# Kernel optimization log

Measured on AMD Instinct MI355X. Metric: run time of the kernel, lower is better.

## Reference

```python
import math
import jax, jax.numpy as jnp
import numpy as np

N, T, D, H, DH = 4, 2048, 1024, 16, 64
CAP = 30.0
EPS = 1e-5


def _layernorm(x, g, b):
    m = jnp.mean(x, axis=-1, keepdims=True)
    v = jnp.mean(jnp.square(x - m), axis=-1, keepdims=True)
    return (x - m) * jax.lax.rsqrt(v + EPS) * g + b


def _rope(x):
    # x: [N, H, t, d]; interleaved rotary (rotary-embedding-torch style), theta=10000
    t, d = x.shape[2], x.shape[3]
    inv_freq = 1.0 / (10000.0 ** (jnp.arange(0, d, 2, dtype=jnp.float32) / d))
    ang = jnp.arange(t, dtype=jnp.float32)[:, None] * inv_freq[None, :]  # [t, d/2]
    cos, sin = jnp.cos(ang), jnp.sin(ang)
    x1, x2 = x[..., 0::2], x[..., 1::2]
    r1 = x1 * cos - x2 * sin
    r2 = x1 * sin + x2 * cos
    return jnp.stack([r1, r2], axis=-1).reshape(x.shape)


def setup_inputs() -> dict:
    key = jax.random.key(0)
    ks = jax.random.split(key, 8)
    s = 0.02
    lengths = jax.random.randint(ks[6], (N,), T // 2, T + 1).astype(jnp.int32)
    key_padding_mask = jnp.arange(T)[None, :] >= lengths[:, None]  # True = pad
    attn_mask = jnp.triu(jnp.ones((T, T), dtype=bool), 1)  # causal: True = masked
    return {
        "x": jax.random.normal(ks[0], (N, T, D), jnp.float32),
        "ln_g": jnp.ones((D,), jnp.float32),
        "ln_b": jnp.zeros((D,), jnp.float32),
        "Wq": jax.random.normal(ks[1], (D, H * DH), jnp.float32) * s,
        "bq": jnp.zeros((H * DH,), jnp.float32),
        "Wk": jax.random.normal(ks[2], (D, H * DH), jnp.float32) * s,
        "bk": jnp.zeros((H * DH,), jnp.float32),
        "Wv": jax.random.normal(ks[3], (D, H * DH), jnp.float32) * s,
        "bv": jnp.zeros((H * DH,), jnp.float32),
        "Wo": jax.random.normal(ks[4], (H * DH, D), jnp.float32) * s,
        "bo": jnp.zeros((D,), jnp.float32),
        "key_padding_mask": key_padding_mask,
        "attn_mask": attn_mask,
        "key_value_sequence_lengths": lengths,
    }


def reference(x, ln_g, ln_b, Wq, bq, Wk, bk, Wv, bv, Wo, bo,
              key_padding_mask, attn_mask, key_value_sequence_lengths):
    n, t, _ = x.shape
    h = _layernorm(x, ln_g, ln_b)  # shared LN for q/k/v (self-attention)
    q = (h @ Wq + bq).reshape(n, t, H, DH).transpose(0, 2, 1, 3)  # [n,H,t,d]
    k = (h @ Wk + bk).reshape(n, t, H, DH).transpose(0, 2, 1, 3)
    v = (h @ Wv + bv).reshape(n, t, H, DH).transpose(0, 2, 1, 3)
    q = _rope(q)
    k = _rope(k)
    scores = jnp.einsum('bhtd,bhTd->bhtT', q, k) / math.sqrt(DH)
    scores = CAP * jnp.tanh(scores / CAP)  # tanh soft-cap
    mask = key_padding_mask[:, None, None, :] | attn_mask[None, None, :, :]
    scores = jnp.where(mask, -jnp.inf, scores)
    attn = jax.nn.softmax(scores, axis=-1)
    out = jnp.einsum('bhtT,bhTd->bhtd', attn, v)
    out = out.transpose(0, 2, 1, 3).reshape(n, t, H * DH)
    return out @ Wo + bo
```

## Files before the change

### kernel.cpp

```cpp
#include <hip/hip_runtime.h>
#include <hip/hip_bf16.h>

typedef unsigned short u16;
typedef unsigned int   u32;
typedef __bf16 bf16x8 __attribute__((ext_vector_type(8)));
typedef float  f32x4  __attribute__((ext_vector_type(4)));

#define NB 4
#define T_ 2048
#define D_ 1024
#define H_ 16
#define DH 64
#define M_ (NB * T_)
#define PSTR 72

__device__ __forceinline__ float bf2f(u16 u) {
    union { u32 i; float f; } v; v.i = ((u32)u) << 16; return v.f;
}
__device__ __forceinline__ u16 f2bf(float f) {
    union { float fl; u32 i; } v; v.fl = f;
    u32 r = v.i + 0x7fff + ((v.i >> 16) & 1);
    return (u16)(r >> 16);
}

__device__ __forceinline__ void gl_lds16(const u16* g, u16* l) {
    __builtin_amdgcn_global_load_lds((const __attribute__((address_space(1))) void*)g,
                                     (__attribute__((address_space(3))) void*)l,
                                     16, 0, 0);
}

__device__ __forceinline__ int detect_f32(const u16* p) {
    int weird = 0;
    const int lane = threadIdx.x & 63;
    #pragma unroll
    for (int i = 0; i < 4; ++i) {
        const u16 u = p[lane * 4 + i];
        const int e = (u >> 7) & 0xFF;
        weird += (e == 0xFF || (e >= 0x01 && e <= 0x3F) || (e >= 0xC0 && e <= 0xFE));
    }
    #pragma unroll
    for (int off = 32; off; off >>= 1) weird += __shfl_xor(weird, off);
    return weird >= 16;
}

__device__ __forceinline__ int read_len(const void* raw, int b) {
    const int* a32 = (const int*)raw;
    bool ok32 = true;
    #pragma unroll
    for (int i = 0; i < NB; ++i) {
        const int v = a32[i];
        if (v < 1 || v > T_) ok32 = false;
    }
    int v = ok32 ? a32[b] : (int)((const long long*)raw)[b];
    return min(max(v, 1), T_);
}

__global__ __launch_bounds__(256) void ln_kernel(const void* __restrict__ xraw,
                                                 const void* __restrict__ graw,
                                                 const void* __restrict__ braw,
                                                 u16* __restrict__ h) {
    const int row = blockIdx.x;
    const int tid = threadIdx.x;
    const int isf = detect_f32((const u16*)xraw);

    float xv[4];
    if (isf) {
        const float* xr = (const float*)xraw + (size_t)row * D_;
        *(float4*)xv = *(const float4*)&xr[tid * 4];
    } else {
        const u16* xr = (const u16*)xraw + (size_t)row * D_;
        u16 loc[4] __attribute__((aligned(8)));
        *(uint2*)loc = *(const uint2*)&xr[tid * 4];
        #pragma unroll
        for (int i = 0; i < 4; ++i) xv[i] = bf2f(loc[i]);
    }

    float s = xv[0] + xv[1] + xv[2] + xv[3];
    float q = xv[0]*xv[0] + xv[1]*xv[1] + xv[2]*xv[2] + xv[3]*xv[3];

    #pragma unroll
    for (int off = 32; off; off >>= 1) {
        s += __shfl_xor(s, off);
        q += __shfl_xor(q, off);
    }
    __shared__ float red[8];
    const int wave = tid >> 6, lane = tid & 63;
    if (lane == 0) { red[wave] = s; red[4 + wave] = q; }
    __syncthreads();
    s = red[0] + red[1] + red[2] + red[3];
    q = red[4] + red[5] + red[6] + red[7];

    const float mean = s * (1.0f / D_);
    const float var  = q * (1.0f / D_) - mean * mean;
    const float rs   = rsqrtf(var + 1e-5f);

    u16 o[4] __attribute__((aligned(8)));
    #pragma unroll
    for (int i = 0; i < 4; ++i) {
        const int c = tid * 4 + i;
        const float gv = isf ? ((const float*)graw)[c] : bf2f(((const u16*)graw)[c]);
        const float bv = isf ? ((const float*)braw)[c] : bf2f(((const u16*)braw)[c]);
        o[i] = f2bf((xv[i] - mean) * rs * gv + bv);
    }
    *(uint2*)&h[(size_t)row * D_ + tid * 4] = *(uint2*)o;
}

__global__ __launch_bounds__(256) void wconv_kernel(const void* __restrict__ Wraw,
                                                    u16* __restrict__ Wt) {
    __shared__ u16 tile[64][PSTR];
    const int isf = detect_f32((const u16*)Wraw);
    const int n0 = blockIdx.x * 64;
    const int k0 = blockIdx.y * 64;
    const int tid = threadIdx.x;
    const int tr  = tid >> 2;
    const int tc  = (tid & 3) * 16;

    if (isf) {
        const float* W = (const float*)Wraw;
        #pragma unroll
        for (int i = 0; i < 16; ++i)
            tile[tc + i][tr] = f2bf(W[(size_t)(k0 + tr) * D_ + n0 + tc + i]);
    } else {
        const u16* W = (const u16*)Wraw;
        #pragma unroll
        for (int i = 0; i < 16; ++i)
            tile[tc + i][tr] = W[(size_t)(k0 + tr) * D_ + n0 + tc + i];
    }
    __syncthreads();
    *(uint4*)&Wt[(size_t)(n0 + tr) * D_ + k0 + tc]     = *(uint4*)&tile[tr][tc];
    *(uint4*)&Wt[(size_t)(n0 + tr) * D_ + k0 + tc + 8] = *(uint4*)&tile[tr][tc + 8];
}

__global__ __launch_bounds__(256) void qkv_kernel(const u16* __restrict__ A,
                                                  const u16* __restrict__ Wt3,
                                                  const void* __restrict__ Braw,
                                                  const void* __restrict__ bqr,
                                                  const void* __restrict__ bkr,
                                                  const void* __restrict__ bvr,
                                                  u16* __restrict__ qo,
                                                  u16* __restrict__ ko,
                                                  u16* __restrict__ vo) {
    __shared__ __align__(16) u16 As[128 * 32];
    __shared__ __align__(16) u16 Bs[128 * 32];

    const int tid   = threadIdx.x;
    const int wave  = tid >> 6;
    const int lane  = tid & 63;
    const int quad  = lane >> 4;
    const int lr    = lane & 15;
    const int ntile = blockIdx.x * 128;
    const int mtile = blockIdx.y * 128;
    const int seg   = ntile >> 10;

    const int isf = detect_f32((const u16*)Braw);

    const int srow = wave * 32 + (lane >> 2);
    const int scol = (lane & 3) * 8;
    const u16* aptr0 = A   + (size_t)(mtile + srow) * D_ + scol;
    const u16* aptr1 = A   + (size_t)(mtile + srow + 16) * D_ + scol;
    const u16* bptr0 = Wt3 + (size_t)(ntile + srow) * D_ + scol;
    const u16* bptr1 = Wt3 + (size_t)(ntile + srow + 16) * D_ + scol;
    u16* alds0 = As + wave * 1024;
    u16* alds1 = As + wave * 1024 + 512;
    u16* blds0 = Bs + wave * 1024;
    u16* blds1 = Bs + wave * 1024 + 512;

    const int mbase = (wave >> 1) * 64;
    const int nbase = (wave & 1) * 64;

    f32x4 acc[4][4];
    #pragma unroll
    for (int m = 0; m < 4; ++m)
        #pragma unroll
        for (int n = 0; n < 4; ++n)
            acc[m][n] = (f32x4){0.f, 0.f, 0.f, 0.f};

    for (int k0 = 0; k0 < D_; k0 += 32) {
        gl_lds16(aptr0 + k0, alds0);
        gl_lds16(aptr1 + k0, alds1);
        gl_lds16(bptr0 + k0, blds0);
        gl_lds16(bptr1 + k0, blds1);
        __syncthreads();

        bf16x8 af[4], bfr[4];
        #pragma unroll
        for (int m = 0; m < 4; ++m)
            af[m] = *(const bf16x8*)&As[(mbase + m * 16 + lr) * 32 + quad * 8];
        #pragma unroll
        for (int n = 0; n < 4; ++n)
            bfr[n] = *(const bf16x8*)&Bs[(nbase + n * 16 + lr) * 32 + quad * 8];
        #pragma unroll
        for (int m = 0; m < 4; ++m)
            #pragma unroll
            for (int n = 0; n < 4; ++n)
                acc[m][n] = __builtin_amdgcn_mfma_f32_16x16x32_bf16(af[m], bfr[n], acc[m][n], 0, 0, 0);

        __syncthreads();
    }

    const void* biasraw = (seg == 0) ? bqr : (seg == 1) ? bkr : bvr;
    u16* out            = (seg == 0) ? qo  : (seg == 1) ? ko  : vo;
    const int nloc = (ntile & 1023) + nbase;

    #pragma unroll
    for (int m = 0; m < 4; ++m) {
        #pragma unroll
        for (int n = 0; n < 4; ++n) {
            const int ncl = nloc + n * 16 + lr;
            const float bv = isf ? ((const float*)biasraw)[ncl]
                                 : bf2f(((const u16*)biasraw)[ncl]);
            #pragma unroll
            for (int r = 0; r < 4; ++r) {
                const int mrow = mtile + mbase + m * 16 + quad * 4 + r;
                float v = acc[m][n][r] + bv;
                const int d  = ncl & (DH - 1);
                const int hh = ncl >> 6;
                const int t  = mrow & (T_ - 1);
                const int bb = mrow >> 11;
                if (seg < 2) {
                    const float other = __shfl_xor(v, 1);
                    const int i = d >> 1;
                    const float inv = exp2f(-(float)i * 0.41524101186092f);
                    const float ang = (float)t * inv;
                    float sv, cv;
                    __sincosf(ang, &sv, &cv);
                    v = (d & 1) ? (other * sv + v * cv) : (v * cv - other * sv);
                    out[(((size_t)(bb * H_ + hh) * T_) + t) * DH + d] = f2bf(v);
                } else {
                    out[(((size_t)(bb * H_ + hh) * DH) + d) * T_ + t] = f2bf(v);
                }
            }
        }
    }
}

__global__ __launch_bounds__(256) void gemm128_kernel(const u16* __restrict__ A,
                                                      const u16* __restrict__ Bt,
                                                      const void* __restrict__ Braw,
                                                      const void* __restrict__ biasraw,
                                                      void* __restrict__ out,
                                                      const int mode) {
    __shared__ __align__(16) u16 As[128 * 32];
    __shared__ __align__(16) u16 Bs[128 * 32];

    const int tid   = threadIdx.x;
    const int wave  = tid >> 6;
    const int lane  = tid & 63;
    const int quad  = lane >> 4;
    const int lr    = lane & 15;
    const int ntile = blockIdx.x * 128;
    const int mtile = blockIdx.y * 128;

    const int isf = detect_f32((const u16*)Braw);

    const int srow = wave * 32 + (lane >> 2);
    const int scol = (lane & 3) * 8;
    const u16* aptr0 = A  + (size_t)(mtile + srow) * D_ + scol;
    const u16* aptr1 = A  + (size_t)(mtile + srow + 16) * D_ + scol;
    const u16* bptr0 = Bt + (size_t)(ntile + srow) * D_ + scol;
    const u16* bptr1 = Bt + (size_t)(ntile + srow + 16) * D_ + scol;
    u16* alds0 = As + wave * 1024;
    u16* alds1 = As + wave * 1024 + 512;
    u16* blds0 = Bs + wave * 1024;
    u16* blds1 = Bs + wave * 1024 + 512;

    const int mbase = (wave >> 1) * 64;
    const int nbase = (wave & 1) * 64;

    f32x4 acc[4][4];
    #pragma unroll
    for (int m = 0; m < 4; ++m)
        #pragma unroll
        for (int n = 0; n < 4; ++n)
            acc[m][n] = (f32x4){0.f, 0.f, 0.f, 0.f};

    for (int k0 = 0; k0 < D_; k0 += 32) {
        gl_lds16(aptr0 + k0, alds0);
        gl_lds16(aptr1 + k0, alds1);
        gl_lds16(bptr0 + k0, blds0);
        gl_lds16(bptr1 + k0, blds1);
        __syncthreads();

        bf16x8 af[4], bfr[4];
        #pragma unroll
        for (int m = 0; m < 4; ++m)
            af[m] = *(const bf16x8*)&As[(mbase + m * 16 + lr) * 32 + quad * 8];
        #pragma unroll
        for (int n = 0; n < 4; ++n)
            bfr[n] = *(const bf16x8*)&Bs[(nbase + n * 16 + lr) * 32 + quad * 8];
        #pragma unroll
        for (int m = 0; m < 4; ++m)
            #pragma unroll
            for (int n = 0; n < 4; ++n)
                acc[m][n] = __builtin_amdgcn_mfma_f32_16x16x32_bf16(af[m], bfr[n], acc[m][n], 0, 0, 0);

        __syncthreads();
    }

    #pragma unroll
    for (int m = 0; m < 4; ++m) {
        #pragma unroll
        for (int n = 0; n < 4; ++n) {
            const int ncol = ntile + nbase + n * 16 + lr;
            const float bv = isf ? ((const float*)biasraw)[ncol]
                                 : bf2f(((const u16*)biasraw)[ncol]);
            #pragma unroll
            for (int r = 0; r < 4; ++r) {
                const int mrow = mtile + mbase + m * 16 + quad * 4 + r;
                float v = acc[m][n][r] + bv;
                if (mode == 2) {
                    const float other = __shfl_xor(v, 1);
                    const int d = ncol & (DH - 1);
                    const int t = mrow & (T_ - 1);
                    const int i = d >> 1;
                    const float inv = exp2f(-(float)i * 0.41524101186092f);
                    const float ang = (float)t * inv;
                    float sv, cv;
                    __sincosf(ang, &sv, &cv);
                    v = (d & 1) ? (other * sv + v * cv) : (v * cv - other * sv);
                }
                const int d  = ncol & (DH - 1);
                const int hh = ncol >> 6;
                const int t  = mrow & (T_ - 1);
                const int bb = mrow >> 11;
                if (mode == 0) {
                    if (isf) ((float*)out)[(size_t)mrow * D_ + ncol] = v;
                    else     ((u16*)out)[(size_t)mrow * D_ + ncol] = f2bf(v);
                } else if (mode == 1) {
                    ((u16*)out)[(((size_t)(bb * H_ + hh) * DH) + d) * T_ + t] = f2bf(v);
                } else {
                    ((u16*)out)[(((size_t)(bb * H_ + hh) * T_) + t) * DH + d] = f2bf(v);
                }
            }
        }
    }
}

__global__ __launch_bounds__(256) void gemm_kernel(const u16* __restrict__ A,
                                                   const void* __restrict__ Braw,
                                                   const u16* __restrict__ Bt,
                                                   const void* __restrict__ biasraw,
                                                   void* __restrict__ out,
                                                   const int mode) {
    __shared__ __align__(16) u16 As[128 * 32];
    __shared__ __align__(16) u16 Bs[64 * 32];

    const int tid   = threadIdx.x;
    const int ntile = blockIdx.x * 64;
    const int mtile = blockIdx.y * 128;
    const int wave  = tid >> 6;
    const int lane  = tid & 63;
    const int quad  = lane >> 4;
    const int lr    = lane & 15;

    const int isf = detect_f32((const u16*)Braw);
    const float* Bf = (const float*)Braw;
    const u16*   Bu = (const u16*)Braw;

    f32x4 acc[2][4];
    #pragma unroll
    for (int s = 0; s < 2; ++s)
        #pragma unroll
        for (int n = 0; n < 4; ++n)
            acc[s][n] = (f32x4){0.f, 0.f, 0.f, 0.f};

    const int ar  = tid >> 1;
    const int akb = (tid & 1) * 16;
    const int bn  = tid & 63;
    const int bkb = (tid >> 6) * 8;
    const u16* Arow = A + (size_t)(mtile + ar) * D_ + akb;
    const size_t bcol0 = (size_t)bkb * D_ + ntile + bn;

    for (int k0 = 0; k0 < D_; k0 += 32) {
        *(uint4*)&As[ar * 32 + akb]     = *(const uint4*)(Arow + k0);
        *(uint4*)&As[ar * 32 + akb + 8] = *(const uint4*)(Arow + k0 + 8);
        {
            u16 tmp[8] __attribute__((aligned(16)));
            if (isf) {
                #pragma unroll
                for (int j = 0; j < 8; ++j) tmp[j] = f2bf(Bf[bcol0 + (size_t)(k0 + j) * D_]);
            } else {
                #pragma unroll
                for (int j = 0; j < 8; ++j) tmp[j] = Bu[bcol0 + (size_t)(k0 + j) * D_];
            }
            *(uint4*)&Bs[bn * 32 + bkb] = *(uint4*)tmp;
        }
        __syncthreads();

        const int mbase = wave * 32;
        bf16x8 af0 = *(const bf16x8*)&As[(mbase +      lr) * 32 + quad * 8];
        bf16x8 af1 = *(const bf16x8*)&As[(mbase + 16 + lr) * 32 + quad * 8];
        #pragma unroll
        for (int nt = 0; nt < 4; ++nt) {
            bf16x8 bf = *(const bf16x8*)&Bs[(nt * 16 + lr) * 32 + quad * 8];
            acc[0][nt] = __builtin_amdgcn_mfma_f32_16x16x32_bf16(af0, bf, acc[0][nt], 0, 0, 0);
            acc[1][nt] = __builtin_amdgcn_mfma_f32_16x16x32_bf16(af1, bf, acc[1][nt], 0, 0, 0);
        }
        __syncthreads();
    }

    #pragma unroll
    for (int s2 = 0; s2 < 2; ++s2) {
        #pragma unroll
        for (int nt = 0; nt < 4; ++nt) {
            const int ncol = ntile + nt * 16 + lr;
            const float bv = isf ? ((const float*)biasraw)[ncol]
                                 : bf2f(((const u16*)biasraw)[ncol]);
            #pragma unroll
            for (int r = 0; r < 4; ++r) {
                const int mrow = mtile + wave * 32 + s2 * 16 + quad * 4 + r;
                float v = acc[s2][nt][r] + bv;
                if (mode == 2) {
                    const float other = __shfl_xor(v, 1);
                    const int d = ncol & (DH - 1);
                    const int t = mrow & (T_ - 1);
                    const int i = d >> 1;
                    const float inv = exp2f(-(float)i * 0.41524101186092f);
                    const float ang = (float)t * inv;
                    const float cv = cosf(ang), sv = sinf(ang);
                    v = (d & 1) ? (other * sv + v * cv) : (v * cv - other * sv);
                }
                const int d  = ncol & (DH - 1);
                const int hh = ncol >> 6;
                const int t  = mrow & (T_ - 1);
                const int bb = mrow >> 11;
                if (mode == 0) {
                    if (isf) ((float*)out)[(size_t)mrow * D_ + ncol] = v;
                    else     ((u16*)out)[(size_t)mrow * D_ + ncol] = f2bf(v);
                } else if (mode == 1) {
                    ((u16*)out)[(((size_t)(bb * H_ + hh) * DH) + d) * T_ + t] = f2bf(v);
                } else {
                    ((u16*)out)[(((size_t)(bb * H_ + hh) * T_) + t) * DH + d] = f2bf(v);
                }
            }
        }
    }
}

__global__ __launch_bounds__(256) void attn_kernel(const u16* __restrict__ Q,
                                                   const u16* __restrict__ K,
                                                   const u16* __restrict__ Vt,
                                                   const void* __restrict__ lensraw,
                                                   u16* __restrict__ ctx) {
    __shared__ __align__(16) u16 Ps[64 * PSTR];
    __shared__ __align__(16) u16 Ks[2][64 * PSTR];
    __shared__ __align__(16) u16 Vts[2][64 * PSTR];

    const int tid  = threadIdx.x;
    const int wave = tid >> 6;
    const int lane = tid & 63;
    const int quad = lane >> 4;
    const int lr   = lane & 15;
    const int bh   = blockIdx.y;
    const int qs   = blockIdx.x * 64;
    const int b    = bh >> 4;
    const int hh   = bh & 15;
    const int len  = read_len(lensraw, b);
    const size_t base = (size_t)bh * T_ * DH;

    const int srow = tid >> 2;
    const int scb  = (tid & 3) * 16;
    const u16* Kb = K + base;
    const u16* Vb = Vt + base;

    *(uint4*)&Ps[srow * PSTR + scb]     = *(const uint4*)&Q[base + (size_t)(qs + srow) * DH + scb];
    *(uint4*)&Ps[srow * PSTR + scb + 8] = *(const uint4*)&Q[base + (size_t)(qs + srow) * DH + scb + 8];
    {
        uint4 k0 = *(const uint4*)&Kb[(size_t)srow * DH + scb];
        uint4 k1 = *(const uint4*)&Kb[(size_t)srow * DH + scb + 8];
        uint4 v0 = *(const uint4*)&Vb[(size_t)srow * T_ + scb];
        uint4 v1 = *(const uint4*)&Vb[(size_t)srow * T_ + scb + 8];
        *(uint4*)&Ks[0][srow * PSTR + scb]      = k0;
        *(uint4*)&Ks[0][srow * PSTR + scb + 8]  = k1;
        *(uint4*)&Vts[0][srow * PSTR + scb]     = v0;
        *(uint4*)&Vts[0][srow * PSTR + scb + 8] = v1;
    }
    __syncthreads();
    const bf16x8 qa0 = *(const bf16x8*)&Ps[(wave * 16 + lr) * PSTR + quad * 8];
    const bf16x8 qa1 = *(const bf16x8*)&Ps[(wave * 16 + lr) * PSTR + 32 + quad * 8];
    __syncthreads();

    f32x4 acc[4];
    float l_loc[4] = {0.f, 0.f, 0.f, 0.f};
    #pragma unroll
    for (int nt = 0; nt < 4; ++nt) acc[nt] = (f32x4){0.f, 0.f, 0.f, 0.f};

    const int smax = min(qs + 63, len - 1);
    const int ktn  = smax / 64 + 1;
    const int prow = wave * 16 + quad * 4;

    int buf = 0;
    uint4 kr0, kr1, vr0, vr1;
    for (int kt = 0; kt < ktn; ++kt) {
        const int ks = kt * 64;
        const bool havenext = (kt + 1 < ktn);

        if (havenext) {
            const int ns = ks + 64;
            kr0 = *(const uint4*)&Kb[(size_t)(ns + srow) * DH + scb];
            kr1 = *(const uint4*)&Kb[(size_t)(ns + srow) * DH + scb + 8];
            vr0 = *(const uint4*)&Vb[(size_t)srow * T_ + ns + scb];
            vr1 = *(const uint4*)&Vb[(size_t)srow * T_ + ns + scb + 8];
        }

        f32x4 s[4];
        #pragma unroll
        for (int nt = 0; nt < 4; ++nt) s[nt] = (f32x4){0.f, 0.f, 0.f, 0.f};
        #pragma unroll
        for (int nt = 0; nt < 4; ++nt) {
            bf16x8 kb0 = *(const bf16x8*)&Ks[buf][(nt * 16 + lr) * PSTR + quad * 8];
            bf16x8 kb1 = *(const bf16x8*)&Ks[buf][(nt * 16 + lr) * PSTR + 32 + quad * 8];
            s[nt] = __builtin_amdgcn_mfma_f32_16x16x32_bf16(qa0, kb0, s[nt], 0, 0, 0);
            s[nt] = __builtin_amdgcn_mfma_f32_16x16x32_bf16(qa1, kb1, s[nt], 0, 0, 0);
        }

        const bool need_mask = (ks == qs) || (ks + 63 >= len);
        if (!need_mask) {
            #pragma unroll
            for (int r = 0; r < 4; ++r) {
                #pragma unroll
                for (int nt = 0; nt < 4; ++nt) {
                    const float z = __expf(s[nt][r] * (1.0f / 120.0f));
                    const float p = __expf(-60.0f * __builtin_amdgcn_rcpf(z + 1.0f));
                    l_loc[r] += p;
                    Ps[(prow + r) * PSTR + nt * 16 + lr] = f2bf(p);
                }
            }
        } else {
            #pragma unroll
            for (int r = 0; r < 4; ++r) {
                const int trow = qs + prow + r;
                #pragma unroll
                for (int nt = 0; nt < 4; ++nt) {
                    const float z = __expf(s[nt][r] * (1.0f / 120.0f));
                    float p = __expf(-60.0f * __builtin_amdgcn_rcpf(z + 1.0f));
                    const int col = ks + nt * 16 + lr;
                    p = (col > trow || col >= len) ? 0.f : p;
                    l_loc[r] += p;
                    Ps[(prow + r) * PSTR + nt * 16 + lr] = f2bf(p);
                }
            }
        }
        __syncthreads();

        bf16x8 pa0 = *(const bf16x8*)&Ps[(wave * 16 + lr) * PSTR + quad * 8];
        bf16x8 pa1 = *(const bf16x8*)&Ps[(wave * 16 + lr) * PSTR + 32 + quad * 8];
        #pragma unroll
        for (int nt = 0; nt < 4; ++nt) {
            bf16x8 vb0 = *(const bf16x8*)&Vts[buf][(nt * 16 + lr) * PSTR + quad * 8];
            bf16x8 vb1 = *(const bf16x8*)&Vts[buf][(nt * 16 + lr) * PSTR + 32 + quad * 8];
            acc[nt] = __builtin_amdgcn_mfma_f32_16x16x32_bf16(pa0, vb0, acc[nt], 0, 0, 0);
            acc[nt] = __builtin_amdgcn_mfma_f32_16x16x32_bf16(pa1, vb1, acc[nt], 0, 0, 0);
        }

        if (havenext) {
            *(uint4*)&Ks[buf ^ 1][srow * PSTR + scb]      = kr0;
            *(uint4*)&Ks[buf ^ 1][srow * PSTR + scb + 8]  = kr1;
            *(uint4*)&Vts[buf ^ 1][srow * PSTR + scb]     = vr0;
            *(uint4*)&Vts[buf ^ 1][srow * PSTR + scb + 8] = vr1;
        }
        __syncthreads();
        buf ^= 1;
    }

    #pragma unroll
    for (int r = 0; r < 4; ++r) {
        float l = l_loc[r];
        #pragma unroll
        for (int off = 1; off < 16; off <<= 1) l += __shfl_xor(l, off);
        const float invl = (l > 0.f) ? (1.0f / l) : 0.f;
        const int qrow = prow + r;
        #pragma unroll
        for (int nt = 0; nt < 4; ++nt) {
            ctx[(size_t)(b * T_ + qs + qrow) * D_ + hh * DH + nt * 16 + lr] =
                f2bf(acc[nt][r] * invl);
        }
    }
}

extern "C" void kernel_launch(void* const* d_in, const int* in_sizes, int n_in,
                              void* d_out, int out_size, void* d_ws, size_t ws_size,
                              hipStream_t stream) {
    u16* h = (u16*)d_ws;
    const size_t MD = (size_t)M_ * D_;
    const size_t WD = (size_t)D_ * D_;
    u16* q  = h + MD;
    u16* k  = q + MD;
    u16* vt = k + MD;
    const bool havewt = ws_size >= (4 * MD + 4 * WD) * sizeof(u16);
    u16* wtq = havewt ? (vt + MD)  : nullptr;
    u16* wtk = havewt ? (wtq + WD) : nullptr;
    u16* wtv = havewt ? (wtk + WD) : nullptr;
    u16* wto = havewt ? (wtv + WD) : nullptr;

    ln_kernel<<<M_, 256, 0, stream>>>(d_in[0], d_in[1], d_in[2], h);

    if (havewt) {
        dim3 wgrid(D_ / 64, D_ / 64);
        wconv_kernel<<<wgrid, 256, 0, stream>>>(d_in[3], wtq);
        wconv_kernel<<<wgrid, 256, 0, stream>>>(d_in[5], wtk);
        wconv_kernel<<<wgrid, 256, 0, stream>>>(d_in[7], wtv);
        wconv_kernel<<<wgrid, 256, 0, stream>>>(d_in[9], wto);

        qkv_kernel<<<dim3(3 * D_ / 128, M_ / 128), 256, 0, stream>>>(
            h, wtq, d_in[3], d_in[4], d_in[6], d_in[8], q, k, vt);

        attn_kernel<<<dim3(T_ / 64, NB * H_), 256, 0, stream>>>(q, k, vt, d_in[13], h);

        gemm128_kernel<<<dim3(D_ / 128, M_ / 128), 256, 0, stream>>>(
            h, wto, d_in[9], d_in[10], d_out, 0);
    } else {
        dim3 ggrid(D_ / 64, M_ / 128);
        gemm_kernel<<<ggrid, 256, 0, stream>>>(h, d_in[3], nullptr, d_in[4], q, 2);
        gemm_kernel<<<ggrid, 256, 0, stream>>>(h, d_in[5], nullptr, d_in[6], k, 2);
        gemm_kernel<<<ggrid, 256, 0, stream>>>(h, d_in[7], nullptr, d_in[8], vt, 1);

        attn_kernel<<<dim3(T_ / 64, NB * H_), 256, 0, stream>>>(q, k, vt, d_in[13], h);

        gemm_kernel<<<ggrid, 256, 0, stream>>>(h, d_in[9], nullptr, d_in[10], d_out, 0);
    }
}
```

Baseline: 400.8 us.

## Write QKV row-major with RoPE table, add V transpose kernel, tune attention loop

```diff
diff --git a/kernel.cpp b/kernel.cpp
--- a/kernel.cpp
+++ b/kernel.cpp
@@ -18,9 +18,8 @@
     union { u32 i; float f; } v; v.i = ((u32)u) << 16; return v.f;
 }
 __device__ __forceinline__ u16 f2bf(float f) {
-    union { float fl; u32 i; } v; v.fl = f;
-    u32 r = v.i + 0x7fff + ((v.i >> 16) & 1);
-    return (u16)(r >> 16);
+    __bf16 b = (__bf16)f;
+    union { __bf16 b; u16 u; } v; v.b = b; return v.u;
 }
 
 __device__ __forceinline__ void gl_lds16(const u16* g, u16* l) {
@@ -131,6 +130,36 @@
     *(uint4*)&Wt[(size_t)(n0 + tr) * D_ + k0 + tc + 8] = *(uint4*)&tile[tr][tc + 8];
 }
 
+__global__ __launch_bounds__(256) void rope_kernel(float2* __restrict__ tab) {
+    const int gid = blockIdx.x * 256 + threadIdx.x;
+    const int t = gid >> 5, i = gid & 31;
+    const float inv = exp2f(-(float)i * 0.41524101186092f);
+    const float ang = (float)t * inv;
+    float sv, cv;
+    sincosf(ang, &sv, &cv);
+    tab[gid] = make_float2(cv, sv);
+}
+
+__global__ __launch_bounds__(256) void vtrans_kernel(const u16* __restrict__ vtmp,
+                                                     u16* __restrict__ vt) {
+    __shared__ u16 tile[64][PSTR];
+    const int bh = blockIdx.y;
+    const int b  = bh >> 4;
+    const int hh = bh & 15;
+    const int t0 = blockIdx.x * 64;
+    const int tid = threadIdx.x;
+    const int tr  = tid >> 2;
+    const int tc  = (tid & 3) * 16;
+
+    #pragma unroll
+    for (int i = 0; i < 16; ++i)
+        tile[tc + i][tr] = vtmp[(size_t)(b * T_ + t0 + tr) * D_ + hh * DH + tc + i];
+    __syncthreads();
+    u16* dst = vt + (size_t)bh * DH * T_ + (size_t)tr * T_ + t0;
+    *(uint4*)&dst[tc]     = *(uint4*)&tile[tr][tc];
+    *(uint4*)&dst[tc + 8] = *(uint4*)&tile[tr][tc + 8];
+}
+
 __global__ __launch_bounds__(256) void qkv_kernel(const u16* __restrict__ A,
                                                   const u16* __restrict__ Wt3,
                                                   const void* __restrict__ Braw,
@@ -139,7 +168,8 @@
                                                   const void* __restrict__ bvr,
                                                   u16* __restrict__ qo,
                                                   u16* __restrict__ ko,
-                                                  u16* __restrict__ vo) {
+                                                  u16* __restrict__ vo,
+                                                  const float2* __restrict__ tab) {
     __shared__ __align__(16) u16 As[128 * 32];
     __shared__ __align__(16) u16 Bs[128 * 32];
 
@@ -213,22 +243,14 @@
             for (int r = 0; r < 4; ++r) {
                 const int mrow = mtile + mbase + m * 16 + quad * 4 + r;
                 float v = acc[m][n][r] + bv;
-                const int d  = ncl & (DH - 1);
-                const int hh = ncl >> 6;
-                const int t  = mrow & (T_ - 1);
-                const int bb = mrow >> 11;
                 if (seg < 2) {
                     const float other = __shfl_xor(v, 1);
-                    const int i = d >> 1;
-                    const float inv = exp2f(-(float)i * 0.41524101186092f);
-                    const float ang = (float)t * inv;
-                    float sv, cv;
-                    __sincosf(ang, &sv, &cv);
-                    v = (d & 1) ? (other * sv + v * cv) : (v * cv - other * sv);
-                    out[(((size_t)(bb * H_ + hh) * T_) + t) * DH + d] = f2bf(v);
-                } else {
-                    out[(((size_t)(bb * H_ + hh) * DH) + d) * T_ + t] = f2bf(v);
+                    const int d = ncl & (DH - 1);
+                    const int t = mrow & (T_ - 1);
+                    const float2 cs = tab[t * 32 + (d >> 1)];
+                    v = (d & 1) ? (other * cs.y + v * cs.x) : (v * cs.x - other * cs.y);
                 }
+                out[(size_t)mrow * D_ + ncl] = f2bf(v);
             }
         }
     }
@@ -338,7 +360,6 @@
 
 __global__ __launch_bounds__(256) void gemm_kernel(const u16* __restrict__ A,
                                                    const void* __restrict__ Braw,
-                                                   const u16* __restrict__ Bt,
                                                    const void* __restrict__ biasraw,
                                                    void* __restrict__ out,
                                                    const int mode) {
@@ -441,7 +462,8 @@
                                                    const u16* __restrict__ K,
                                                    const u16* __restrict__ Vt,
                                                    const void* __restrict__ lensraw,
-                                                   u16* __restrict__ ctx) {
+                                                   u16* __restrict__ ctx,
+                                                   const int rowmajor) {
     __shared__ __align__(16) u16 Ps[64 * PSTR];
     __shared__ __align__(16) u16 Ks[2][64 * PSTR];
     __shared__ __align__(16) u16 Vts[2][64 * PSTR];
@@ -456,18 +478,22 @@
     const int b    = bh >> 4;
     const int hh   = bh & 15;
     const int len  = read_len(lensraw, b);
-    const size_t base = (size_t)bh * T_ * DH;
+
+    const size_t qkstride = rowmajor ? (size_t)D_ : (size_t)DH;
+    const size_t qkoff    = rowmajor ? ((size_t)b * T_ * D_ + hh * DH)
+                                     : ((size_t)bh * T_ * DH);
+    const u16* Qp = Q + qkoff;
+    const u16* Kp = K + qkoff;
+    const u16* Vb = Vt + (size_t)bh * DH * T_;
 
     const int srow = tid >> 2;
     const int scb  = (tid & 3) * 16;
-    const u16* Kb = K + base;
-    const u16* Vb = Vt + base;
-
-    *(uint4*)&Ps[srow * PSTR + scb]     = *(const uint4*)&Q[base + (size_t)(qs + srow) * DH + scb];
-    *(uint4*)&Ps[srow * PSTR + scb + 8] = *(const uint4*)&Q[base + (size_t)(qs + srow) * DH + scb + 8];
+
+    *(uint4*)&Ps[srow * PSTR + scb]     = *(const uint4*)&Qp[(size_t)(qs + srow) * qkstride + scb];
+    *(uint4*)&Ps[srow * PSTR + scb + 8] = *(const uint4*)&Qp[(size_t)(qs + srow) * qkstride + scb + 8];
     {
-        uint4 k0 = *(const uint4*)&Kb[(size_t)srow * DH + scb];
-        uint4 k1 = *(const uint4*)&Kb[(size_t)srow * DH + scb + 8];
+        uint4 k0 = *(const uint4*)&Kp[(size_t)srow * qkstride + scb];
+        uint4 k1 = *(const uint4*)&Kp[(size_t)srow * qkstride + scb + 8];
         uint4 v0 = *(const uint4*)&Vb[(size_t)srow * T_ + scb];
         uint4 v1 = *(const uint4*)&Vb[(size_t)srow * T_ + scb + 8];
         *(uint4*)&Ks[0][srow * PSTR + scb]      = k0;
@@ -478,7 +504,6 @@
     __syncthreads();
     const bf16x8 qa0 = *(const bf16x8*)&Ps[(wave * 16 + lr) * PSTR + quad * 8];
     const bf16x8 qa1 = *(const bf16x8*)&Ps[(wave * 16 + lr) * PSTR + 32 + quad * 8];
-    __syncthreads();
 
     f32x4 acc[4];
     float l_loc[4] = {0.f, 0.f, 0.f, 0.f};
@@ -488,6 +513,9 @@
     const int smax = min(qs + 63, len - 1);
     const int ktn  = smax / 64 + 1;
     const int prow = wave * 16 + quad * 4;
+
+    const float C1 = 1.44269504f / 120.0f;
+    const float C2 = -60.0f * 1.44269504f;
 
     int buf = 0;
     uint4 kr0, kr1, vr0, vr1;
@@ -497,8 +525,8 @@
 
         if (havenext) {
             const int ns = ks + 64;
-            kr0 = *(const uint4*)&Kb[(size_t)(ns + srow) * DH + scb];
-            kr1 = *(const uint4*)&Kb[(size_t)(ns + srow) * DH + scb + 8];
+            kr0 = *(const uint4*)&Kp[(size_t)(ns + srow) * qkstride + scb];
+            kr1 = *(const uint4*)&Kp[(size_t)(ns + srow) * qkstride + scb + 8];
             vr0 = *(const uint4*)&Vb[(size_t)srow * T_ + ns + scb];
             vr1 = *(const uint4*)&Vb[(size_t)srow * T_ + ns + scb + 8];
         }
@@ -506,6 +534,7 @@
         f32x4 s[4];
         #pragma unroll
         for (int nt = 0; nt < 4; ++nt) s[nt] = (f32x4){0.f, 0.f, 0.f, 0.f};
+        __builtin_amdgcn_s_setprio(1);
         #pragma unroll
         for (int nt = 0; nt < 4; ++nt) {
             bf16x8 kb0 = *(const bf16x8*)&Ks[buf][(nt * 16 + lr) * PSTR + quad * 8];
@@ -513,6 +542,7 @@
             s[nt] = __builtin_amdgcn_mfma_f32_16x16x32_bf16(qa0, kb0, s[nt], 0, 0, 0);
             s[nt] = __builtin_amdgcn_mfma_f32_16x16x32_bf16(qa1, kb1, s[nt], 0, 0, 0);
         }
+        __builtin_amdgcn_s_setprio(0);
 
         const bool need_mask = (ks == qs) || (ks + 63 >= len);
         if (!need_mask) {
@@ -520,8 +550,8 @@
             for (int r = 0; r < 4; ++r) {
                 #pragma unroll
                 for (int nt = 0; nt < 4; ++nt) {
-                    const float z = __expf(s[nt][r] * (1.0f / 120.0f));
-                    const float p = __expf(-60.0f * __builtin_amdgcn_rcpf(z + 1.0f));
+                    const float z = exp2f(s[nt][r] * C1);
+                    const float p = exp2f(C2 * __builtin_amdgcn_rcpf(z + 1.0f));
                     l_loc[r] += p;
                     Ps[(prow + r) * PSTR + nt * 16 + lr] = f2bf(p);
                 }
@@ -532,8 +562,8 @@
                 const int trow = qs + prow + r;
                 #pragma unroll
                 for (int nt = 0; nt < 4; ++nt) {
-                    const float z = __expf(s[nt][r] * (1.0f / 120.0f));
-                    float p = __expf(-60.0f * __builtin_amdgcn_rcpf(z + 1.0f));
+                    const float z = exp2f(s[nt][r] * C1);
+                    float p = exp2f(C2 * __builtin_amdgcn_rcpf(z + 1.0f));
                     const int col = ks + nt * 16 + lr;
                     p = (col > trow || col >= len) ? 0.f : p;
                     l_loc[r] += p;
@@ -541,10 +571,10 @@
                 }
             }
         }
-        __syncthreads();
 
         bf16x8 pa0 = *(const bf16x8*)&Ps[(wave * 16 + lr) * PSTR + quad * 8];
         bf16x8 pa1 = *(const bf16x8*)&Ps[(wave * 16 + lr) * PSTR + 32 + quad * 8];
+        __builtin_amdgcn_s_setprio(1);
         #pragma unroll
         for (int nt = 0; nt < 4; ++nt) {
             bf16x8 vb0 = *(const bf16x8*)&Vts[buf][(nt * 16 + lr) * PSTR + quad * 8];
@@ -552,6 +582,7 @@
             acc[nt] = __builtin_amdgcn_mfma_f32_16x16x32_bf16(pa0, vb0, acc[nt], 0, 0, 0);
             acc[nt] = __builtin_amdgcn_mfma_f32_16x16x32_bf16(pa1, vb1, acc[nt], 0, 0, 0);
         }
+        __builtin_amdgcn_s_setprio(0);
 
         if (havenext) {
             *(uint4*)&Ks[buf ^ 1][srow * PSTR + scb]      = kr0;
@@ -587,36 +618,58 @@
     u16* q  = h + MD;
     u16* k  = q + MD;
     u16* vt = k + MD;
-    const bool havewt = ws_size >= (4 * MD + 4 * WD) * sizeof(u16);
+    const bool havewt  = ws_size >= (4 * MD + 4 * WD) * sizeof(u16);
+    const bool havebig = ws_size >= (5 * MD + 4 * WD) * sizeof(u16)
+                                    + (size_t)T_ * 32 * sizeof(float2);
     u16* wtq = havewt ? (vt + MD)  : nullptr;
     u16* wtk = havewt ? (wtq + WD) : nullptr;
     u16* wtv = havewt ? (wtk + WD) : nullptr;
     u16* wto = havewt ? (wtv + WD) : nullptr;
+    u16* vtmp = havebig ? (wto + WD) : nullptr;
+    float2* tab = havebig ? (float2*)(vtmp + MD) : nullptr;
 
     ln_kernel<<<M_, 256, 0, stream>>>(d_in[0], d_in[1], d_in[2], h);
 
-    if (havewt) {
+    if (havebig) {
         dim3 wgrid(D_ / 64, D_ / 64);
         wconv_kernel<<<wgrid, 256, 0, stream>>>(d_in[3], wtq);
         wconv_kernel<<<wgrid, 256, 0, stream>>>(d_in[5], wtk);
         wconv_kernel<<<wgrid, 256, 0, stream>>>(d_in[7], wtv);
         wconv_kernel<<<wgrid, 256, 0, stream>>>(d_in[9], wto);
+        rope_kernel<<<256, 256, 0, stream>>>(tab);
 
         qkv_kernel<<<dim3(3 * D_ / 128, M_ / 128), 256, 0, stream>>>(
-            h, wtq, d_in[3], d_in[4], d_in[6], d_in[8], q, k, vt);
-
-        attn_kernel<<<dim3(T_ / 64, NB * H_), 256, 0, stream>>>(q, k, vt, d_in[13], h);
+            h, wtq, d_in[3], d_in[4], d_in[6], d_in[8], q, k, vtmp, tab);
+
+        vtrans_kernel<<<dim3(T_ / 64, NB * H_), 256, 0, stream>>>(vtmp, vt);
+
+        attn_kernel<<<dim3(T_ / 64, NB * H_), 256, 0, stream>>>(q, k, vt, d_in[13], h, 1);
 
         gemm128_kernel<<<dim3(D_ / 128, M_ / 128), 256, 0, stream>>>(
             h, wto, d_in[9], d_in[10], d_out, 0);
+    } else if (havewt) {
+        dim3 wgrid(D_ / 64, D_ / 64);
+        wconv_kernel<<<wgrid, 256, 0, stream>>>(d_in[3], wtq);
+        wconv_kernel<<<wgrid, 256, 0, stream>>>(d_in[5], wtk);
+        wconv_kernel<<<wgrid, 256, 0, stream>>>(d_in[7], wtv);
+        wconv_kernel<<<wgrid, 256, 0, stream>>>(d_in[9], wto);
+
+        dim3 g128(D_ / 128, M_ / 128);
+        gemm128_kernel<<<g128, 256, 0, stream>>>(h, wtq, d_in[3], d_in[4], q, 2);
+        gemm128_kernel<<<g128, 256, 0, stream>>>(h, wtk, d_in[5], d_in[6], k, 2);
+        gemm128_kernel<<<g128, 256, 0, stream>>>(h, wtv, d_in[7], d_in[8], vt, 1);
+
+        attn_kernel<<<dim3(T_ / 64, NB * H_), 256, 0, stream>>>(q, k, vt, d_in[13], h, 0);
+
+        gemm128_kernel<<<g128, 256, 0, stream>>>(h, wto, d_in[9], d_in[10], d_out, 0);
     } else {
         dim3 ggrid(D_ / 64, M_ / 128);
-        gemm_kernel<<<ggrid, 256, 0, stream>>>(h, d_in[3], nullptr, d_in[4], q, 2);
-        gemm_kernel<<<ggrid, 256, 0, stream>>>(h, d_in[5], nullptr, d_in[6], k, 2);
-        gemm_kernel<<<ggrid, 256, 0, stream>>>(h, d_in[7], nullptr, d_in[8], vt, 1);
-
-        attn_kernel<<<dim3(T_ / 64, NB * H_), 256, 0, stream>>>(q, k, vt, d_in[13], h);
-
-        gemm_kernel<<<ggrid, 256, 0, stream>>>(h, d_in[9], nullptr, d_in[10], d_out, 0);
-    }
-}
+        gemm_kernel<<<ggrid, 256, 0, stream>>>(h, d_in[3], d_in[4], q, 2);
+        gemm_kernel<<<ggrid, 256, 0, stream>>>(h, d_in[5], d_in[6], k, 2);
+        gemm_kernel<<<ggrid, 256, 0, stream>>>(h, d_in[7], d_in[8], vt, 1);
+
+        attn_kernel<<<dim3(T_ / 64, NB * H_), 256, 0, stream>>>(q, k, vt, d_in[13], h, 0);
+
+        gemm_kernel<<<ggrid, 256, 0, stream>>>(h, d_in[9], d_in[10], d_out, 0);
+    }
+}
```

New measurement: 435.0 us. 1.09x slower.
